# Performance work log

Hardware: AMD Instinct MI355X
Metric: run time of the kernel (lower is better)

The kernel has to match this reference:

```python
import jax, jax.numpy as jnp
import numpy as np

N_QUBITS = 4
N_LAYERS = 6
BATCH = 524288
C64 = jnp.complex64


def setup_inputs() -> dict:
    key = jax.random.key(0)
    k1, k2, k3 = jax.random.split(key, 3)
    x = jax.random.normal(k1, (BATCH, N_QUBITS), dtype=jnp.float32)
    weights = jax.random.normal(k2, (N_LAYERS, N_QUBITS, 3), dtype=jnp.float32)
    bias = jax.random.normal(k3, (3,), dtype=jnp.float32)
    class_bias = jnp.zeros((1,), dtype=jnp.float32)
    return {"x": x, "weights": weights, "bias": bias, "class_bias": class_bias}


def _rx(t):
    # RX(t) = [[cos(t/2), -i sin(t/2)], [-i sin(t/2), cos(t/2)]]
    c = jnp.cos(0.5 * t)
    s = jnp.sin(0.5 * t)
    return jnp.stack([jnp.stack([c + 0j, -1j * s]), jnp.stack([-1j * s, c + 0j])]).astype(C64)


def _ry(t):
    # RY(t) = [[cos, -sin], [sin, cos]] (real)
    c = jnp.cos(0.5 * t)
    s = jnp.sin(0.5 * t)
    return jnp.stack([jnp.stack([c, -s]), jnp.stack([s, c])]).astype(C64)


def _rz(t):
    # RZ(t) = diag(exp(-i t/2), exp(+i t/2))
    e = jnp.exp(-0.5j * t).astype(C64)
    return jnp.diag(jnp.stack([e, jnp.conj(e)]))


def _apply_1q(psi, U, q):
    # psi: [B,2,2,2,2]; contract 2x2 U into qubit axis (1+q)
    ax = 1 + q
    out = jnp.tensordot(U, psi, axes=([1], [ax]))  # [2, B, ...]
    return jnp.moveaxis(out, 0, ax)


def _cnot(psi, ctrl, tgt):
    ax_c, ax_t = 1 + ctrl, 1 + tgt
    a0 = jax.lax.index_in_dim(psi, 0, ax_c, keepdims=True)
    a1 = jnp.flip(jax.lax.index_in_dim(psi, 1, ax_c, keepdims=True), axis=ax_t)
    return jnp.concatenate([a0, a1], axis=ax_c)


def _circuit(x, weights):
    # AngleEmbedding (RX rotations) on |0000>: per-qubit amps [cos(x/2), -i sin(x/2)]
    half = 0.5 * x
    c = jnp.cos(half)
    s = jnp.sin(half)
    a = jnp.stack([c.astype(C64), (-1j * s).astype(C64)], axis=-1)  # [B, nq, 2]
    psi = jnp.einsum('bi,bj,bk,bl->bijkl', a[:, 0], a[:, 1], a[:, 2], a[:, 3])
    for layer in range(N_LAYERS):
        for cw, tw in ((0, 1), (1, 2), (2, 3), (3, 0)):
            psi = _cnot(psi, cw, tw)
        for q in range(N_QUBITS):
            psi = _apply_1q(psi, _rx(weights[layer, q, 0]), q)
            psi = _apply_1q(psi, _ry(weights[layer, q, 1]), q)
            psi = _apply_1q(psi, _rz(weights[layer, q, 2]), q)
    p = psi.real ** 2 + psi.imag ** 2  # probabilities [B,2,2,2,2]
    z = jnp.array([1.0, -1.0], dtype=jnp.float32)
    evs = jnp.stack([
        jnp.einsum('bijkl,i->b', p, z),
        jnp.einsum('bijkl,j->b', p, z),
        jnp.einsum('bijkl,k->b', p, z),
        jnp.einsum('bijkl,l->b', p, z),
    ], axis=-1)  # [B, 4], matches torch.stack(res).permute(1,0)
    return evs


def reference(x, weights, bias, class_bias):
    # bias / class_bias are parameters of the original module but are never
    # used inside the quantum circuit; output depends only on x and weights.
    return _circuit(x, weights)
```

## Files before the change

### kernel.cpp

```cpp
#include <hip/hip_runtime.h>
#include <math.h>

#define NQ 4
#define NL 6
#define BATCH 524288
#define EPT 2
#define LP 17
#define NBLK (BATCH / (256 * EPT))

struct C2 { float re, im; };

__device__ __forceinline__ C2 cmul(C2 a, C2 b) {
    return C2{ __builtin_fmaf(a.re, b.re, -a.im * b.im),
               __builtin_fmaf(a.re, b.im,  a.im * b.re) };
}

__global__ __launch_bounds__(256, 4) void qone2_kernel(const float4* __restrict__ x,
                                                       const float* __restrict__ w,
                                                       float4* __restrict__ out) {
    __shared__ float  sU[NL * NQ * 8];
    __shared__ float2 sL[NL][16 * LP];
    __shared__ float2 sP[3][16 * LP];
    __shared__ float2 sDm[16 * LP];
    __shared__ float4 sV4[128];

    const int tid = threadIdx.x;
    const int base = blockIdx.x * (256 * EPT) + tid;

    float m[EPT][16];
#pragma unroll
    for (int e = 0; e < EPT; ++e) {
        const float4 xv = x[base + e * 256];
        float c0, s0, c1, s1, c2, s2, c3, s3;
        __sincosf(0.5f * xv.x, &s0, &c0);
        __sincosf(0.5f * xv.y, &s1, &c1);
        __sincosf(0.5f * xv.z, &s2, &c2);
        __sincosf(0.5f * xv.w, &s3, &c3);
        float ab[4];
        ab[0] = c0 * c1; ab[1] = c0 * s1; ab[2] = s0 * c1; ab[3] = s0 * s1;
        float abc[8];
#pragma unroll
        for (int k = 0; k < 4; ++k) { abc[2 * k] = ab[k] * c2; abc[2 * k + 1] = ab[k] * s2; }
#pragma unroll
        for (int k = 0; k < 8; ++k) { m[e][2 * k] = abc[k] * c3; m[e][2 * k + 1] = abc[k] * s3; }
    }

    if (tid < NL * NQ) {
        const float a = w[tid * 3 + 0];
        const float b = w[tid * 3 + 1];
        const float g = w[tid * 3 + 2];
        float ca, sa, cb, sb, cg, sg;
        sincosf(0.5f * a, &sa, &ca);
        sincosf(0.5f * b, &sb, &cb);
        sincosf(0.5f * g, &sg, &cg);
        C2 M00{cb * ca,  sb * sa};
        C2 M01{-sb * ca, -cb * sa};
        C2 M10{sb * ca,  -cb * sa};
        C2 M11{cb * ca,  -sb * sa};
        C2 em{cg, -sg}, ep{cg, sg};
        C2 U00 = cmul(em, M00), U01 = cmul(em, M01);
        C2 U10 = cmul(ep, M10), U11 = cmul(ep, M11);
        float* o = &sU[tid * 8];
        o[0] = U00.re; o[1] = U00.im; o[2] = U01.re; o[3] = U01.im;
        o[4] = U10.re; o[5] = U10.im; o[6] = U11.re; o[7] = U11.im;
    }
    __syncthreads();

    const int r = tid >> 4;
    const int c = tid & 15;

    {
        int b0 = (c >> 3) & 1, b1 = (c >> 2) & 1, b2 = (c >> 1) & 1, b3 = c & 1;
        b1 ^= b0; b2 ^= b1; b3 ^= b2; b0 ^= b3;
        const int r0 = (r >> 3) & 1, r1 = (r >> 2) & 1, r2 = (r >> 1) & 1, r3 = r & 1;
        const int o0 = (r0 * 2 + b0) * 2;
        const int o1 = (r1 * 2 + b1) * 2;
        const int o2 = (r2 * 2 + b2) * 2;
        const int o3 = (r3 * 2 + b3) * 2;
#pragma unroll
        for (int l = 0; l < NL; ++l) {
            const float* g = &sU[l * 32];
            C2 a{g[o0], g[o0 + 1]};
            a = cmul(a, C2{g[8  + o1], g[8  + o1 + 1]});
            a = cmul(a, C2{g[16 + o2], g[16 + o2 + 1]});
            a = cmul(a, C2{g[24 + o3], g[24 + o3 + 1]});
            sL[l][r * LP + c] = make_float2(a.re, a.im);
        }
    }
    __syncthreads();

#pragma unroll
    for (int s = 0; s < 3; ++s) {
        float re = 0.f, im = 0.f;
#pragma unroll
        for (int k = 0; k < 16; ++k) {
            const float2 xk = sL[2 * s + 1][r * LP + k];
            const float2 yk = sL[2 * s][k * LP + c];
            re = __builtin_fmaf(xk.x, yk.x, re); re = __builtin_fmaf(-xk.y, yk.y, re);
            im = __builtin_fmaf(xk.x, yk.y, im); im = __builtin_fmaf( xk.y, yk.x, im);
        }
        sP[s][r * LP + c] = make_float2(re, im);
    }
    __syncthreads();

    {
        float re = 0.f, im = 0.f;
#pragma unroll
        for (int k = 0; k < 16; ++k) {
            const float2 xk = sP[1][r * LP + k];
            const float2 yk = sP[0][k * LP + c];
            re = __builtin_fmaf(xk.x, yk.x, re); re = __builtin_fmaf(-xk.y, yk.y, re);
            im = __builtin_fmaf(xk.x, yk.y, im); im = __builtin_fmaf( xk.y, yk.x, im);
        }
        sDm[r * LP + c] = make_float2(re, im);
    }
    __syncthreads();

    {
        float re = 0.f, im = 0.f;
#pragma unroll
        for (int k = 0; k < 16; ++k) {
            const float2 xk = sP[2][r * LP + k];
            const float2 yk = sDm[k * LP + c];
            re = __builtin_fmaf(xk.x, yk.x, re); re = __builtin_fmaf(-xk.y, yk.y, re);
            im = __builtin_fmaf(xk.x, yk.y, im); im = __builtin_fmaf( xk.y, yk.x, im);
        }
        const int p4 = __popc(c) & 3;
        float wr, wi;
        if      (p4 == 0) { wr = re;  wi = im;  }
        else if (p4 == 1) { wr = im;  wi = -re; }
        else if (p4 == 2) { wr = -re; wi = -im; }
        else              { wr = -im; wi = re;  }
        float* sVf = reinterpret_cast<float*>(sV4);
        reinterpret_cast<float2*>(&sVf[r * 32 + 2 * c])[0] = make_float2(wr, wi);
    }
    __syncthreads();

    float ev[EPT][4];
#pragma unroll
    for (int e = 0; e < EPT; ++e)
#pragma unroll
        for (int q = 0; q < 4; ++q) ev[e][q] = 0.f;

#pragma unroll
    for (int rr = 0; rr < 16; ++rr) {
        float4 row[8];
#pragma unroll
        for (int k = 0; k < 8; ++k) row[k] = sV4[rr * 8 + k];
#pragma unroll
        for (int e = 0; e < EPT; ++e) {
            float re = 0.f, im = 0.f;
#pragma unroll
            for (int k = 0; k < 8; ++k) {
                re = __builtin_fmaf(m[e][2 * k],     row[k].x, re);
                im = __builtin_fmaf(m[e][2 * k],     row[k].y, im);
                re = __builtin_fmaf(m[e][2 * k + 1], row[k].z, re);
                im = __builtin_fmaf(m[e][2 * k + 1], row[k].w, im);
            }
            const float p = __builtin_fmaf(re, re, im * im);
            if (rr & 8) ev[e][0] -= p; else ev[e][0] += p;
            if (rr & 4) ev[e][1] -= p; else ev[e][1] += p;
            if (rr & 2) ev[e][2] -= p; else ev[e][2] += p;
            if (rr & 1) ev[e][3] -= p; else ev[e][3] += p;
        }
    }

#pragma unroll
    for (int e = 0; e < EPT; ++e) {
        out[base + e * 256] = make_float4(ev[e][0], ev[e][1], ev[e][2], ev[e][3]);
    }
}

extern "C" void kernel_launch(void* const* d_in, const int* in_sizes, int n_in,
                              void* d_out, int out_size, void* d_ws, size_t ws_size,
                              hipStream_t stream) {
    const float4* x = (const float4*)d_in[0];
    const float*  w = (const float*)d_in[1];
    float4* out = (float4*)d_out;

    qone2_kernel<<<NBLK, 256, 0, stream>>>(x, w, out);
}
```

Before: 23.77 us.

## Apply final unitary via split-bf16 MFMA over persistent wave-tiled batch loop

Replaces the per-thread scalar 16x16 complex matrix-vector product with bf16 MFMA 16x16x32 instructions. Each wave handles 16 samples per tile, and hi/lo bf16 splitting of both operands approximates fp32 accuracy. The grid becomes a persistent 512-block launch with a grid-stride tile loop and next-x prefetch, so the per-block unitary construction is amortized over many samples instead of repeated for 512 samples per block. The cost is wave-level shuffle reductions, bf16 conversion work, and possible accuracy loss from the three-term split product.

```diff
diff --git a/kernel.cpp b/kernel.cpp
--- a/kernel.cpp
+++ b/kernel.cpp
@@ -4,9 +4,14 @@
 #define NQ 4
 #define NL 6
 #define BATCH 524288
-#define EPT 2
 #define LP 17
-#define NBLK (BATCH / (256 * EPT))
+#define NTILE (BATCH / 16)
+#define NBLK 512
+#define WPB 4
+#define NWAVE (NBLK * WPB)
+
+typedef __attribute__((ext_vector_type(8))) short bf16x8;
+typedef __attribute__((ext_vector_type(4))) float f32x4;
 
 struct C2 { float re, im; };
 
@@ -15,35 +20,25 @@
                __builtin_fmaf(a.re, b.im,  a.im * b.re) };
 }
 
-__global__ __launch_bounds__(256, 4) void qone2_kernel(const float4* __restrict__ x,
+__device__ __forceinline__ unsigned short f2bf(float f) {
+    unsigned u = __float_as_uint(f);
+    u = u + 0x7FFFu + ((u >> 16) & 1u);
+    return (unsigned short)(u >> 16);
+}
+__device__ __forceinline__ float bf2f(unsigned short b) {
+    return __uint_as_float(((unsigned)b) << 16);
+}
+
+__global__ __launch_bounds__(256, 4) void qmfma_kernel(const float4* __restrict__ x,
                                                        const float* __restrict__ w,
                                                        float4* __restrict__ out) {
     __shared__ float  sU[NL * NQ * 8];
     __shared__ float2 sL[NL][16 * LP];
     __shared__ float2 sP[3][16 * LP];
     __shared__ float2 sDm[16 * LP];
-    __shared__ float4 sV4[128];
+    __shared__ float  sVf[16 * 32];
 
     const int tid = threadIdx.x;
-    const int base = blockIdx.x * (256 * EPT) + tid;
-
-    float m[EPT][16];
-#pragma unroll
-    for (int e = 0; e < EPT; ++e) {
-        const float4 xv = x[base + e * 256];
-        float c0, s0, c1, s1, c2, s2, c3, s3;
-        __sincosf(0.5f * xv.x, &s0, &c0);
-        __sincosf(0.5f * xv.y, &s1, &c1);
-        __sincosf(0.5f * xv.z, &s2, &c2);
-        __sincosf(0.5f * xv.w, &s3, &c3);
-        float ab[4];
-        ab[0] = c0 * c1; ab[1] = c0 * s1; ab[2] = s0 * c1; ab[3] = s0 * s1;
-        float abc[8];
-#pragma unroll
-        for (int k = 0; k < 4; ++k) { abc[2 * k] = ab[k] * c2; abc[2 * k + 1] = ab[k] * s2; }
-#pragma unroll
-        for (int k = 0; k < 8; ++k) { m[e][2 * k] = abc[k] * c3; m[e][2 * k + 1] = abc[k] * s3; }
-    }
 
     if (tid < NL * NQ) {
         const float a = w[tid * 3 + 0];
@@ -66,10 +61,8 @@
     }
     __syncthreads();
 
-    const int r = tid >> 4;
-    const int c = tid & 15;
-
-    {
+    {
+        const int r = tid >> 4, c = tid & 15;
         int b0 = (c >> 3) & 1, b1 = (c >> 2) & 1, b2 = (c >> 1) & 1, b3 = c & 1;
         b1 ^= b0; b2 ^= b1; b3 ^= b2; b0 ^= b3;
         const int r0 = (r >> 3) & 1, r1 = (r >> 2) & 1, r2 = (r >> 1) & 1, r3 = r & 1;
@@ -89,21 +82,24 @@
     }
     __syncthreads();
 
-#pragma unroll
-    for (int s = 0; s < 3; ++s) {
-        float re = 0.f, im = 0.f;
-#pragma unroll
-        for (int k = 0; k < 16; ++k) {
-            const float2 xk = sL[2 * s + 1][r * LP + k];
-            const float2 yk = sL[2 * s][k * LP + c];
-            re = __builtin_fmaf(xk.x, yk.x, re); re = __builtin_fmaf(-xk.y, yk.y, re);
-            im = __builtin_fmaf(xk.x, yk.y, im); im = __builtin_fmaf( xk.y, yk.x, im);
-        }
-        sP[s][r * LP + c] = make_float2(re, im);
-    }
-    __syncthreads();
-
-    {
+    {
+        const int r = tid >> 4, c = tid & 15;
+#pragma unroll
+        for (int s = 0; s < 3; ++s) {
+            float re = 0.f, im = 0.f;
+#pragma unroll
+            for (int k = 0; k < 16; ++k) {
+                const float2 xk = sL[2 * s + 1][r * LP + k];
+                const float2 yk = sL[2 * s][k * LP + c];
+                re = __builtin_fmaf(xk.x, yk.x, re); re = __builtin_fmaf(-xk.y, yk.y, re);
+                im = __builtin_fmaf(xk.x, yk.y, im); im = __builtin_fmaf( xk.y, yk.x, im);
+            }
+            sP[s][r * LP + c] = make_float2(re, im);
+        }
+    }
+    __syncthreads();
+    {
+        const int r = tid >> 4, c = tid & 15;
         float re = 0.f, im = 0.f;
 #pragma unroll
         for (int k = 0; k < 16; ++k) {
@@ -115,8 +111,8 @@
         sDm[r * LP + c] = make_float2(re, im);
     }
     __syncthreads();
-
-    {
+    {
+        const int r = tid >> 4, c = tid & 15;
         float re = 0.f, im = 0.f;
 #pragma unroll
         for (int k = 0; k < 16; ++k) {
@@ -131,43 +127,89 @@
         else if (p4 == 1) { wr = im;  wi = -re; }
         else if (p4 == 2) { wr = -re; wi = -im; }
         else              { wr = -im; wi = re;  }
-        float* sVf = reinterpret_cast<float*>(sV4);
         reinterpret_cast<float2*>(&sVf[r * 32 + 2 * c])[0] = make_float2(wr, wi);
     }
     __syncthreads();
 
-    float ev[EPT][4];
-#pragma unroll
-    for (int e = 0; e < EPT; ++e)
-#pragma unroll
-        for (int q = 0; q < 4; ++q) ev[e][q] = 0.f;
-
-#pragma unroll
-    for (int rr = 0; rr < 16; ++rr) {
-        float4 row[8];
-#pragma unroll
-        for (int k = 0; k < 8; ++k) row[k] = sV4[rr * 8 + k];
-#pragma unroll
-        for (int e = 0; e < EPT; ++e) {
-            float re = 0.f, im = 0.f;
-#pragma unroll
-            for (int k = 0; k < 8; ++k) {
-                re = __builtin_fmaf(m[e][2 * k],     row[k].x, re);
-                im = __builtin_fmaf(m[e][2 * k],     row[k].y, im);
-                re = __builtin_fmaf(m[e][2 * k + 1], row[k].z, re);
-                im = __builtin_fmaf(m[e][2 * k + 1], row[k].w, im);
-            }
-            const float p = __builtin_fmaf(re, re, im * im);
-            if (rr & 8) ev[e][0] -= p; else ev[e][0] += p;
-            if (rr & 4) ev[e][1] -= p; else ev[e][1] += p;
-            if (rr & 2) ev[e][2] -= p; else ev[e][2] += p;
-            if (rr & 1) ev[e][3] -= p; else ev[e][3] += p;
-        }
-    }
-
-#pragma unroll
-    for (int e = 0; e < EPT; ++e) {
-        out[base + e * 256] = make_float4(ev[e][0], ev[e][1], ev[e][2], ev[e][3]);
+    const int l  = tid & 63;
+    const int rA = l & 15;
+    const int g  = l >> 4;
+    const int gh = g & 1;
+    bf16x8 A1re, A1im, A2re, A2im;
+#pragma unroll
+    for (int j = 0; j < 8; ++j) {
+        const int c = 8 * gh + j;
+        const float vr = sVf[rA * 32 + 2 * c];
+        const float vi = sVf[rA * 32 + 2 * c + 1];
+        const unsigned short hr = f2bf(vr), hi_ = f2bf(vi);
+        if (g < 2) {
+            A1re[j] = (short)hr;  A1im[j] = (short)hi_;
+            A2re[j] = (short)hr;  A2im[j] = (short)hi_;
+        } else {
+            A1re[j] = (short)f2bf(vr - bf2f(hr));
+            A1im[j] = (short)f2bf(vi - bf2f(hi_));
+            A2re[j] = 0;          A2im[j] = 0;
+        }
+    }
+
+    const int wg = (blockIdx.x << 2) + (tid >> 6);
+    const int e  = l & 15;
+    const float sgn0 = (g & 2) ? -1.f : 1.f;
+    const float sgn1 = (g & 1) ? -1.f : 1.f;
+
+    int t = wg;
+    float4 xv = x[t * 16 + e];
+    while (t < NTILE) {
+        const int tn = t + NWAVE;
+        float4 xnext = xv;
+        if (tn < NTILE) xnext = x[tn * 16 + e];
+
+        float c0, s0, c1, s1, c2, s2, c3, s3;
+        __sincosf(0.5f * xv.x, &s0, &c0);
+        __sincosf(0.5f * xv.y, &s1, &c1);
+        __sincosf(0.5f * xv.z, &s2, &c2);
+        __sincosf(0.5f * xv.w, &s3, &c3);
+
+        const float f0 = gh ? s0 : c0;
+        const float t0 = f0 * c1, t1 = f0 * s1;
+        const float u0 = t0 * c2, u1 = t0 * s2, u2 = t1 * c2, u3 = t1 * s2;
+        float mv[8];
+        mv[0] = u0 * c3; mv[1] = u0 * s3; mv[2] = u1 * c3; mv[3] = u1 * s3;
+        mv[4] = u2 * c3; mv[5] = u2 * s3; mv[6] = u3 * c3; mv[7] = u3 * s3;
+
+        bf16x8 B1, B2;
+#pragma unroll
+        for (int j = 0; j < 8; ++j) {
+            const unsigned short h = f2bf(mv[j]);
+            B1[j] = (short)h;
+            B2[j] = (short)f2bf(mv[j] - bf2f(h));
+        }
+
+        f32x4 dre = {0.f, 0.f, 0.f, 0.f}, dim = {0.f, 0.f, 0.f, 0.f};
+        dre = __builtin_amdgcn_mfma_f32_16x16x32_bf16(A1re, B1, dre, 0, 0, 0);
+        dre = __builtin_amdgcn_mfma_f32_16x16x32_bf16(A2re, B2, dre, 0, 0, 0);
+        dim = __builtin_amdgcn_mfma_f32_16x16x32_bf16(A1im, B1, dim, 0, 0, 0);
+        dim = __builtin_amdgcn_mfma_f32_16x16x32_bf16(A2im, B2, dim, 0, 0, 0);
+
+        const float p0 = __builtin_fmaf(dre[0], dre[0], dim[0] * dim[0]);
+        const float p1 = __builtin_fmaf(dre[1], dre[1], dim[1] * dim[1]);
+        const float p2 = __builtin_fmaf(dre[2], dre[2], dim[2] * dim[2]);
+        const float p3 = __builtin_fmaf(dre[3], dre[3], dim[3] * dim[3]);
+        const float a_ = p0 + p1, b_ = p2 + p3;
+        float v0 = sgn0 * (a_ + b_);
+        float v1 = sgn1 * (a_ + b_);
+        float v2 = a_ - b_;
+        float v3 = (p0 - p1) + (p2 - p3);
+
+        v0 += __shfl_xor(v0, 16); v1 += __shfl_xor(v1, 16);
+        v2 += __shfl_xor(v2, 16); v3 += __shfl_xor(v3, 16);
+        v0 += __shfl_xor(v0, 32); v1 += __shfl_xor(v1, 32);
+        v2 += __shfl_xor(v2, 32); v3 += __shfl_xor(v3, 32);
+
+        if (l < 16) out[t * 16 + e] = make_float4(v0, v1, v2, v3);
+
+        t = tn;
+        xv = xnext;
     }
 }
 
@@ -178,5 +220,5 @@
     const float*  w = (const float*)d_in[1];
     float4* out = (float4*)d_out;
 
-    qone2_kernel<<<NBLK, 256, 0, stream>>>(x, w, out);
-}
+    qmfma_kernel<<<NBLK, 256, 0, stream>>>(x, w, out);
+}
```

Result: faster. 21.56 us (-9.3%).
